# Performance work log

Measured on AMD Instinct MI355X. Metric: run time of the kernel, lower is better.

The kernel has to match this reference:

```python
import jax, jax.numpy as jnp
import numpy as np

HEAD_DIM = 64
KERNEL_EPS = 1e-3  # lucidrains generalized_kernel kernel_epsilon


def setup_inputs() -> dict:
    key = jax.random.key(0)
    k1, k2, k3, k4 = jax.random.split(key, 4)
    B, H, N, D, R = 4, 8, 4096, HEAD_DIM, 256
    return {
        "Q": jax.random.normal(k1, (B, H, N, D), dtype=jnp.float32),
        "K": jax.random.normal(k2, (B, H, N, D), dtype=jnp.float32),
        "V": jax.random.normal(k3, (B, H, N, D), dtype=jnp.float32),
        "mask": jnp.ones((B, N), dtype=jnp.float32),
        "proj": jax.random.normal(k4, (R, D), dtype=jnp.float32),
    }


def reference(Q, K, V, mask, proj):
    # PerformerAttention.forward: scale Q,K by d^{-1/4}, zero out masked keys/values
    scale = 1.0 / jnp.sqrt(jnp.sqrt(jnp.float32(HEAD_DIM)))
    m = mask[:, None, :, None]               # [B,1,N,1]
    q = Q * scale
    k = K * scale * m
    v = V * m

    # generalized random-feature map phi(x) = relu(x @ proj^T) + eps  -> [B,H,N,R]
    phi_q = jax.nn.relu(jnp.einsum('bhnd,rd->bhnr', q, proj)) + KERNEL_EPS
    phi_k = jax.nn.relu(jnp.einsum('bhnd,rd->bhnr', k, proj)) + KERNEL_EPS

    # non-causal linear attention: out = phi_q (phi_k^T v) / (phi_q (phi_k^T 1))
    k_sum = phi_k.sum(axis=2)                                  # [B,H,R]
    d_inv = 1.0 / jnp.einsum('bhnr,bhr->bhn', phi_q, k_sum)    # [B,H,N]
    context = jnp.einsum('bhnr,bhnd->bhrd', phi_k, v)          # [B,H,R,D]
    out = jnp.einsum('bhnr,bhrd->bhnd', phi_q, context) * d_inv[..., None]
    return out
```

## Files before the change

### kernel.cpp

```cpp
#include <hip/hip_runtime.h>
#include <hip/hip_bf16.h>

#define BB 4
#define HH 8
#define NN 4096
#define DD 64
#define RR 256

constexpr float SCALE = 0.35355339059327373f;
constexpr float KEPS  = 0.001f;

typedef __attribute__((ext_vector_type(8)))  short short8;
typedef __attribute__((ext_vector_type(16))) float f32x16;

#define MFMA(a, b, c) __builtin_amdgcn_mfma_f32_32x32x16_bf16(a, b, c, 0, 0, 0)

union S8U { short8 s; uint4 u; };

__device__ inline unsigned bfpk(float a, float b) {
    __hip_bfloat162 h = __float22bfloat162_rn(make_float2(a, b));
    return *reinterpret_cast<unsigned*>(&h);
}
__device__ inline f32x16 fz16() {
    f32x16 z;
#pragma unroll
    for (int e = 0; e < 16; ++e) z[e] = 0.f;
    return z;
}

__global__ __launch_bounds__(256)
void prep_proj(const float* __restrict__ proj, unsigned short* __restrict__ projb)
{
    const int i = (blockIdx.x * 256 + threadIdx.x) * 4;
    const float4 v = *(const float4*)(proj + i);
    uint2 o; o.x = bfpk(v.x * SCALE, v.y * SCALE); o.y = bfpk(v.z * SCALE, v.w * SCALE);
    *(uint2*)(projb + i) = o;
}

__global__ __launch_bounds__(256, 2)
void pk_ctx_kernel(const float* __restrict__ Kmat, const float* __restrict__ Vmat,
                   const float* __restrict__ mask, const unsigned short* __restrict__ projb,
                   float* __restrict__ g_ctxT, float* __restrict__ g_ksum)
{
    __shared__ unsigned short kt[2][32 * 72];
    __shared__ unsigned short vt[2][32 * 68];

    const int tid = threadIdx.x;
    const int w = tid >> 6, lane = tid & 63;
    const int l31 = lane & 31, hf = lane >> 5;
    const int b = blockIdx.z, h = blockIdx.y;
    const int bh = b * HH + h;
    const int n0 = blockIdx.x * 256;

    const int sn = tid >> 3, sc = (tid & 7) * 8;
    const long rowbase = ((long)bh * NN + n0 + sn) * DD + sc;
    const int  mbase   = b * NN + n0 + sn;

    short8 pfrag[2][4];
#pragma unroll
    for (int rt = 0; rt < 2; ++rt)
#pragma unroll
        for (int ks = 0; ks < 4; ++ks)
            pfrag[rt][ks] = *(const short8*)(projb + (w * 64 + rt * 32 + l31) * DD + ks * 16 + hf * 8);

    f32x16 acc[2][2];
    acc[0][0] = fz16(); acc[0][1] = fz16(); acc[1][0] = fz16(); acc[1][1] = fz16();
    float ksum[2] = {0.f, 0.f};

    auto stage = [&](int buf, int sub) {
        const long off = rowbase + (long)sub * 32 * DD;
        const float m = mask[mbase + sub * 32];
        const float4 ka = *(const float4*)(Kmat + off);
        const float4 kc = *(const float4*)(Kmat + off + 4);
        S8U t; t.u = make_uint4(bfpk(ka.x * m, ka.y * m), bfpk(ka.z * m, ka.w * m),
                                bfpk(kc.x * m, kc.y * m), bfpk(kc.z * m, kc.w * m));
        *(short8*)&kt[buf][sn * 72 + sc] = t.s;
        const float4 va = *(const float4*)(Vmat + off);
        const float4 vc = *(const float4*)(Vmat + off + 4);
        *(uint2*)&vt[buf][sn * 68 + sc]     = make_uint2(bfpk(va.x * m, va.y * m), bfpk(va.z * m, va.w * m));
        *(uint2*)&vt[buf][sn * 68 + sc + 4] = make_uint2(bfpk(vc.x * m, vc.y * m), bfpk(vc.z * m, vc.w * m));
    };

    stage(0, 0);
    __syncthreads();

    for (int sub = 0; sub < 8; ++sub) {
        const int buf = sub & 1;
        if (sub < 7) stage(buf ^ 1, sub + 1);

        short8 afr[4];
#pragma unroll
        for (int ks = 0; ks < 4; ++ks)
            afr[ks] = *(const short8*)&kt[buf][l31 * 72 + ks * 16 + hf * 8];

        unsigned own[2][8];
#pragma unroll
        for (int rt = 0; rt < 2; ++rt) {
            f32x16 p = fz16();
#pragma unroll
            for (int ks = 0; ks < 4; ++ks) p = MFMA(afr[ks], pfrag[rt][ks], p);
#pragma unroll
            for (int g = 0; g < 4; ++g) {
                const float p0 = fmaxf(p[4*g+0], 0.f) + KEPS;
                const float p1 = fmaxf(p[4*g+1], 0.f) + KEPS;
                const float p2 = fmaxf(p[4*g+2], 0.f) + KEPS;
                const float p3 = fmaxf(p[4*g+3], 0.f) + KEPS;
                ksum[rt] += (p0 + p1) + (p2 + p3);
                own[rt][2*g]   = bfpk(p0, p1);
                own[rt][2*g+1] = bfpk(p2, p3);
            }
        }
        unsigned par[2][8];
#pragma unroll
        for (int rt = 0; rt < 2; ++rt)
#pragma unroll
            for (int q = 0; q < 8; ++q)
                par[rt][q] = (unsigned)__shfl_xor((int)own[rt][q], 32, 64);

#pragma unroll
        for (int kk = 0; kk < 2; ++kk) {
            S8U bf[2];
#pragma unroll
            for (int rt = 0; rt < 2; ++rt) {
                if (hf == 0) bf[rt].u = make_uint4(own[rt][4*kk],   own[rt][4*kk+1],
                                                   par[rt][4*kk],   par[rt][4*kk+1]);
                else         bf[rt].u = make_uint4(par[rt][4*kk+2], par[rt][4*kk+3],
                                                   own[rt][4*kk+2], own[rt][4*kk+3]);
            }
#pragma unroll
            for (int mt = 0; mt < 2; ++mt) {
                short8 av;
#pragma unroll
                for (int j = 0; j < 8; ++j)
                    av[j] = (short)vt[buf][(kk * 16 + hf * 8 + j) * 68 + mt * 32 + l31];
                acc[mt][0] = MFMA(av, bf[0].s, acc[mt][0]);
                acc[mt][1] = MFMA(av, bf[1].s, acc[mt][1]);
            }
        }
        __syncthreads();
    }

#pragma unroll
    for (int mt = 0; mt < 2; ++mt)
#pragma unroll
        for (int rt = 0; rt < 2; ++rt)
#pragma unroll
            for (int i = 0; i < 16; ++i) {
                const int drow = mt * 32 + (i & 3) + 8 * (i >> 2) + 4 * hf;
                atomicAdd(g_ctxT + ((long)bh * DD + drow) * RR + w * 64 + rt * 32 + l31,
                          acc[mt][rt][i]);
            }
#pragma unroll
    for (int rt = 0; rt < 2; ++rt) {
        const float kst = ksum[rt] + __shfl_xor(ksum[rt], 32, 64);
        if (hf == 0) atomicAdd(g_ksum + bh * RR + w * 64 + rt * 32 + l31, kst);
    }
}

__global__ __launch_bounds__(256)
void finalize_ctx(const float* __restrict__ g_ctxT, unsigned short* __restrict__ ctb)
{
    const long i = ((long)blockIdx.x * 256 + threadIdx.x) * 8;
    const float4 a = *(const float4*)(g_ctxT + i);
    const float4 c = *(const float4*)(g_ctxT + i + 4);
    uint4 o = make_uint4(bfpk(a.x, a.y), bfpk(a.z, a.w), bfpk(c.x, c.y), bfpk(c.z, c.w));
    *(uint4*)(ctb + i) = o;
}

__global__ __launch_bounds__(256, 4)
void out_kernel(const float* __restrict__ Qmat, const unsigned short* __restrict__ projb,
                const unsigned short* __restrict__ ctb, const float* __restrict__ g_ksum,
                float* __restrict__ out)
{
    __shared__ unsigned short pl[256 * 72];
    __shared__ float ks_lds[RR];

    const int tid = threadIdx.x;
    const int w = tid >> 6, lane = tid & 63;
    const int l31 = lane & 31, hf = lane >> 5;
    const int bh = blockIdx.z * HH + blockIdx.y;
    const int n0 = blockIdx.x * 128;
    const int nl = w * 32 + l31;

#pragma unroll
    for (int t = 0; t < 8; ++t) {
        const int u = tid + t * 256;
        const uint4 v = ((const uint4*)projb)[u];
        *(uint4*)&pl[(u >> 3) * 72 + (u & 7) * 8] = v;
    }
    ks_lds[tid] = g_ksum[bh * RR + tid];

    const long qrow = ((long)bh * NN + n0 + nl) * DD;
    short8 qfr[4];
#pragma unroll
    for (int ks = 0; ks < 4; ++ks) {
        const float4 a = *(const float4*)(Qmat + qrow + ks * 16 + hf * 8);
        const float4 c = *(const float4*)(Qmat + qrow + ks * 16 + hf * 8 + 4);
        S8U t; t.u = make_uint4(bfpk(a.x, a.y), bfpk(a.z, a.w), bfpk(c.x, c.y), bfpk(c.z, c.w));
        qfr[ks] = t.s;
    }
    __syncthreads();

    f32x16 cacc[2];
    cacc[0] = fz16(); cacc[1] = fz16();
    float s_acc = 0.f;

    short8 cpre[4];
#pragma unroll
    for (int q = 0; q < 4; ++q)
        cpre[q] = *(const short8*)(ctb + ((long)bh * DD + (q & 1) * 32 + l31) * RR
                                       + (q >> 1) * 16 + hf * 8);

    for (int rt = 0; rt < 8; ++rt) {
        short8 cur[4];
#pragma unroll
        for (int q = 0; q < 4; ++q) cur[q] = cpre[q];
        if (rt < 7) {
#pragma unroll
            for (int q = 0; q < 4; ++q)
                cpre[q] = *(const short8*)(ctb + ((long)bh * DD + (q & 1) * 32 + l31) * RR
                                               + (rt + 1) * 32 + (q >> 1) * 16 + hf * 8);
        }
        f32x16 p = fz16();
#pragma unroll
        for (int ks = 0; ks < 4; ++ks) {
            const short8 af = *(const short8*)&pl[(rt * 32 + l31) * 72 + ks * 16 + hf * 8];
            p = MFMA(af, qfr[ks], p);
        }
        unsigned own[8];
#pragma unroll
        for (int g = 0; g < 4; ++g) {
            const float4 kv = *(const float4*)&ks_lds[rt * 32 + 8 * g + 4 * hf];
            const float p0 = fmaxf(p[4*g+0], 0.f) + KEPS; s_acc = fmaf(p0, kv.x, s_acc);
            const float p1 = fmaxf(p[4*g+1], 0.f) + KEPS; s_acc = fmaf(p1, kv.y, s_acc);
            const float p2 = fmaxf(p[4*g+2], 0.f) + KEPS; s_acc = fmaf(p2, kv.z, s_acc);
            const float p3 = fmaxf(p[4*g+3], 0.f) + KEPS; s_acc = fmaf(p3, kv.w, s_acc);
            own[2*g]   = bfpk(p0, p1);
            own[2*g+1] = bfpk(p2, p3);
        }
        unsigned par[8];
#pragma unroll
        for (int q = 0; q < 8; ++q) par[q] = (unsigned)__shfl_xor((int)own[q], 32, 64);
#pragma unroll
        for (int kk = 0; kk < 2; ++kk) {
            S8U a;
            if (hf == 0) a.u = make_uint4(own[4*kk],   own[4*kk+1], par[4*kk],   par[4*kk+1]);
            else         a.u = make_uint4(par[4*kk+2], par[4*kk+3], own[4*kk+2], own[4*kk+3]);
            cacc[0] = MFMA(a.s, cur[kk * 2 + 0], cacc[0]);
            cacc[1] = MFMA(a.s, cur[kk * 2 + 1], cacc[1]);
        }
    }

    const float st = s_acc + __shfl_xor(s_acc, 32, 64);
    const float sinv = 1.0f / st;
#pragma unroll
    for (int i = 0; i < 16; ++i) {
        const int row = (i & 3) + 8 * (i >> 2) + 4 * hf;
        const float sv = __shfl(sinv, row, 64);
#pragma unroll
        for (int dt = 0; dt < 2; ++dt)
            out[((long)bh * NN + n0 + w * 32 + row) * DD + dt * 32 + l31] = cacc[dt][i] * sv;
    }
}

extern "C" void kernel_launch(void* const* d_in, const int* in_sizes, int n_in,
                              void* d_out, int out_size, void* d_ws, size_t ws_size,
                              hipStream_t stream)
{
    const float* Q    = (const float*)d_in[0];
    const float* K    = (const float*)d_in[1];
    const float* V    = (const float*)d_in[2];
    const float* mask = (const float*)d_in[3];
    const float* proj = (const float*)d_in[4];
    float* out = (float*)d_out;

    float* g_ctxT = (float*)d_ws;
    float* g_ksum = g_ctxT + (size_t)BB * HH * DD * RR;
    unsigned short* projb = (unsigned short*)(g_ksum + (size_t)BB * HH * RR);
    unsigned short* ctb   = projb + (size_t)RR * DD;

    const size_t zbytes = ((size_t)BB * HH * DD * RR + (size_t)BB * HH * RR) * sizeof(float);
    hipMemsetAsync(d_ws, 0, zbytes, stream);

    prep_proj<<<dim3(RR * DD / 1024), 256, 0, stream>>>(proj, projb);

    dim3 g1(NN / 256, HH, BB);
    pk_ctx_kernel<<<g1, 256, 0, stream>>>(K, V, mask, projb, g_ctxT, g_ksum);

    finalize_ctx<<<dim3(BB * HH * DD * RR / 2048), 256, 0, stream>>>(g_ctxT, ctb);

    dim3 g2(NN / 128, HH, BB);
    out_kernel<<<g2, 256, 0, stream>>>(Q, projb, ctb, g_ksum, out);
}
```

Baseline: 221.5 us.

## Split feature dimension across blocks and drop context finalize kernel

The context kernel now splits the 256 random features into two halves across twice as many blocks, so each wave handles one 32-feature tile. This reduces per-thread registers and raises the occupancy target, at the cost of loading and converting K/V twice. The separate bf16 finalize kernel is removed: the output kernel reads fp32 context directly from global memory and converts it inline. The output kernel also reads proj from global instead of staging it in LDS. Together these aim to cut launch overhead and LDS traffic, but they add redundant global loads and conversions in the inner loop.

```diff
diff --git a/kernel.cpp b/kernel.cpp
--- a/kernel.cpp
+++ b/kernel.cpp
@@ -37,7 +37,7 @@
     *(uint2*)(projb + i) = o;
 }
 
-__global__ __launch_bounds__(256, 2)
+__global__ __launch_bounds__(256, 3)
 void pk_ctx_kernel(const float* __restrict__ Kmat, const float* __restrict__ Vmat,
                    const float* __restrict__ mask, const unsigned short* __restrict__ projb,
                    float* __restrict__ g_ctxT, float* __restrict__ g_ksum)
@@ -50,22 +50,22 @@
     const int l31 = lane & 31, hf = lane >> 5;
     const int b = blockIdx.z, h = blockIdx.y;
     const int bh = b * HH + h;
-    const int n0 = blockIdx.x * 256;
+    const int nc = blockIdx.x >> 1, rhalf = blockIdx.x & 1;
+    const int n0 = nc * 256;
+    const int rg = rhalf * 128 + w * 32 + l31;
 
     const int sn = tid >> 3, sc = (tid & 7) * 8;
     const long rowbase = ((long)bh * NN + n0 + sn) * DD + sc;
     const int  mbase   = b * NN + n0 + sn;
 
-    short8 pfrag[2][4];
-#pragma unroll
-    for (int rt = 0; rt < 2; ++rt)
-#pragma unroll
-        for (int ks = 0; ks < 4; ++ks)
-            pfrag[rt][ks] = *(const short8*)(projb + (w * 64 + rt * 32 + l31) * DD + ks * 16 + hf * 8);
-
-    f32x16 acc[2][2];
-    acc[0][0] = fz16(); acc[0][1] = fz16(); acc[1][0] = fz16(); acc[1][1] = fz16();
-    float ksum[2] = {0.f, 0.f};
+    short8 pfrag[4];
+#pragma unroll
+    for (int ks = 0; ks < 4; ++ks)
+        pfrag[ks] = *(const short8*)(projb + rg * DD + ks * 16 + hf * 8);
+
+    f32x16 acc[2];
+    acc[0] = fz16(); acc[1] = fz16();
+    float ksum = 0.f;
 
     auto stage = [&](int buf, int sub) {
         const long off = rowbase + (long)sub * 32 * DD;
@@ -92,49 +92,37 @@
 #pragma unroll
         for (int ks = 0; ks < 4; ++ks)
             afr[ks] = *(const short8*)&kt[buf][l31 * 72 + ks * 16 + hf * 8];
-
-        unsigned own[2][8];
-#pragma unroll
-        for (int rt = 0; rt < 2; ++rt) {
-            f32x16 p = fz16();
-#pragma unroll
-            for (int ks = 0; ks < 4; ++ks) p = MFMA(afr[ks], pfrag[rt][ks], p);
-#pragma unroll
-            for (int g = 0; g < 4; ++g) {
-                const float p0 = fmaxf(p[4*g+0], 0.f) + KEPS;
-                const float p1 = fmaxf(p[4*g+1], 0.f) + KEPS;
-                const float p2 = fmaxf(p[4*g+2], 0.f) + KEPS;
-                const float p3 = fmaxf(p[4*g+3], 0.f) + KEPS;
-                ksum[rt] += (p0 + p1) + (p2 + p3);
-                own[rt][2*g]   = bfpk(p0, p1);
-                own[rt][2*g+1] = bfpk(p2, p3);
-            }
-        }
-        unsigned par[2][8];
-#pragma unroll
-        for (int rt = 0; rt < 2; ++rt)
-#pragma unroll
-            for (int q = 0; q < 8; ++q)
-                par[rt][q] = (unsigned)__shfl_xor((int)own[rt][q], 32, 64);
+        f32x16 p = fz16();
+#pragma unroll
+        for (int ks = 0; ks < 4; ++ks) p = MFMA(afr[ks], pfrag[ks], p);
+
+        unsigned own[8];
+#pragma unroll
+        for (int g = 0; g < 4; ++g) {
+            const float p0 = fmaxf(p[4*g+0], 0.f) + KEPS;
+            const float p1 = fmaxf(p[4*g+1], 0.f) + KEPS;
+            const float p2 = fmaxf(p[4*g+2], 0.f) + KEPS;
+            const float p3 = fmaxf(p[4*g+3], 0.f) + KEPS;
+            ksum += (p0 + p1) + (p2 + p3);
+            own[2*g]   = bfpk(p0, p1);
+            own[2*g+1] = bfpk(p2, p3);
+        }
+        unsigned par[8];
+#pragma unroll
+        for (int q = 0; q < 8; ++q) par[q] = (unsigned)__shfl_xor((int)own[q], 32, 64);
 
 #pragma unroll
         for (int kk = 0; kk < 2; ++kk) {
-            S8U bf[2];
-#pragma unroll
-            for (int rt = 0; rt < 2; ++rt) {
-                if (hf == 0) bf[rt].u = make_uint4(own[rt][4*kk],   own[rt][4*kk+1],
-                                                   par[rt][4*kk],   par[rt][4*kk+1]);
-                else         bf[rt].u = make_uint4(par[rt][4*kk+2], par[rt][4*kk+3],
-                                                   own[rt][4*kk+2], own[rt][4*kk+3]);
-            }
+            S8U bf;
+            if (hf == 0) bf.u = make_uint4(own[4*kk],   own[4*kk+1], par[4*kk],   par[4*kk+1]);
+            else         bf.u = make_uint4(par[4*kk+2], par[4*kk+3], own[4*kk+2], own[4*kk+3]);
 #pragma unroll
             for (int mt = 0; mt < 2; ++mt) {
                 short8 av;
 #pragma unroll
                 for (int j = 0; j < 8; ++j)
                     av[j] = (short)vt[buf][(kk * 16 + hf * 8 + j) * 68 + mt * 32 + l31];
-                acc[mt][0] = MFMA(av, bf[0].s, acc[mt][0]);
-                acc[mt][1] = MFMA(av, bf[1].s, acc[mt][1]);
+                acc[mt] = MFMA(av, bf.s, acc[mt]);
             }
         }
         __syncthreads();
@@ -143,36 +131,20 @@
 #pragma unroll
     for (int mt = 0; mt < 2; ++mt)
 #pragma unroll
-        for (int rt = 0; rt < 2; ++rt)
-#pragma unroll
-            for (int i = 0; i < 16; ++i) {
-                const int drow = mt * 32 + (i & 3) + 8 * (i >> 2) + 4 * hf;
-                atomicAdd(g_ctxT + ((long)bh * DD + drow) * RR + w * 64 + rt * 32 + l31,
-                          acc[mt][rt][i]);
-            }
-#pragma unroll
-    for (int rt = 0; rt < 2; ++rt) {
-        const float kst = ksum[rt] + __shfl_xor(ksum[rt], 32, 64);
-        if (hf == 0) atomicAdd(g_ksum + bh * RR + w * 64 + rt * 32 + l31, kst);
-    }
-}
-
-__global__ __launch_bounds__(256)
-void finalize_ctx(const float* __restrict__ g_ctxT, unsigned short* __restrict__ ctb)
-{
-    const long i = ((long)blockIdx.x * 256 + threadIdx.x) * 8;
-    const float4 a = *(const float4*)(g_ctxT + i);
-    const float4 c = *(const float4*)(g_ctxT + i + 4);
-    uint4 o = make_uint4(bfpk(a.x, a.y), bfpk(a.z, a.w), bfpk(c.x, c.y), bfpk(c.z, c.w));
-    *(uint4*)(ctb + i) = o;
-}
-
-__global__ __launch_bounds__(256, 4)
+        for (int i = 0; i < 16; ++i) {
+            const int drow = mt * 32 + (i & 3) + 8 * (i >> 2) + 4 * hf;
+            atomicAdd(g_ctxT + ((long)bh * DD + drow) * RR + rhalf * 128 + w * 32 + l31,
+                      acc[mt][i]);
+        }
+    const float kst = ksum + __shfl_xor(ksum, 32, 64);
+    if (hf == 0) atomicAdd(g_ksum + bh * RR + rhalf * 128 + w * 32 + l31, kst);
+}
+
+__global__ __launch_bounds__(256, 3)
 void out_kernel(const float* __restrict__ Qmat, const unsigned short* __restrict__ projb,
-                const unsigned short* __restrict__ ctb, const float* __restrict__ g_ksum,
+                const float* __restrict__ g_ctxT, const float* __restrict__ g_ksum,
                 float* __restrict__ out)
 {
-    __shared__ unsigned short pl[256 * 72];
     __shared__ float ks_lds[RR];
 
     const int tid = threadIdx.x;
@@ -182,12 +154,6 @@
     const int n0 = blockIdx.x * 128;
     const int nl = w * 32 + l31;
 
-#pragma unroll
-    for (int t = 0; t < 8; ++t) {
-        const int u = tid + t * 256;
-        const uint4 v = ((const uint4*)projb)[u];
-        *(uint4*)&pl[(u >> 3) * 72 + (u & 7) * 8] = v;
-    }
     ks_lds[tid] = g_ksum[bh * RR + tid];
 
     const long qrow = ((long)bh * NN + n0 + nl) * DD;
@@ -205,26 +171,11 @@
     cacc[0] = fz16(); cacc[1] = fz16();
     float s_acc = 0.f;
 
-    short8 cpre[4];
-#pragma unroll
-    for (int q = 0; q < 4; ++q)
-        cpre[q] = *(const short8*)(ctb + ((long)bh * DD + (q & 1) * 32 + l31) * RR
-                                       + (q >> 1) * 16 + hf * 8);
-
     for (int rt = 0; rt < 8; ++rt) {
-        short8 cur[4];
-#pragma unroll
-        for (int q = 0; q < 4; ++q) cur[q] = cpre[q];
-        if (rt < 7) {
-#pragma unroll
-            for (int q = 0; q < 4; ++q)
-                cpre[q] = *(const short8*)(ctb + ((long)bh * DD + (q & 1) * 32 + l31) * RR
-                                               + (rt + 1) * 32 + (q >> 1) * 16 + hf * 8);
-        }
         f32x16 p = fz16();
 #pragma unroll
         for (int ks = 0; ks < 4; ++ks) {
-            const short8 af = *(const short8*)&pl[(rt * 32 + l31) * 72 + ks * 16 + hf * 8];
+            const short8 af = *(const short8*)(projb + (rt * 32 + l31) * DD + ks * 16 + hf * 8);
             p = MFMA(af, qfr[ks], p);
         }
         unsigned own[8];
@@ -241,13 +192,22 @@
         unsigned par[8];
 #pragma unroll
         for (int q = 0; q < 8; ++q) par[q] = (unsigned)__shfl_xor((int)own[q], 32, 64);
+
 #pragma unroll
         for (int kk = 0; kk < 2; ++kk) {
             S8U a;
             if (hf == 0) a.u = make_uint4(own[4*kk],   own[4*kk+1], par[4*kk],   par[4*kk+1]);
             else         a.u = make_uint4(par[4*kk+2], par[4*kk+3], own[4*kk+2], own[4*kk+3]);
-            cacc[0] = MFMA(a.s, cur[kk * 2 + 0], cacc[0]);
-            cacc[1] = MFMA(a.s, cur[kk * 2 + 1], cacc[1]);
+#pragma unroll
+            for (int dt = 0; dt < 2; ++dt) {
+                const float* cp = g_ctxT + ((long)bh * DD + dt * 32 + l31) * RR
+                                         + rt * 32 + kk * 16 + hf * 8;
+                const float4 x = *(const float4*)cp;
+                const float4 y = *(const float4*)(cp + 4);
+                S8U bfr; bfr.u = make_uint4(bfpk(x.x, x.y), bfpk(x.z, x.w),
+                                            bfpk(y.x, y.y), bfpk(y.z, y.w));
+                cacc[dt] = MFMA(a.s, bfr.s, cacc[dt]);
+            }
         }
     }
 
@@ -277,18 +237,15 @@
     float* g_ctxT = (float*)d_ws;
     float* g_ksum = g_ctxT + (size_t)BB * HH * DD * RR;
     unsigned short* projb = (unsigned short*)(g_ksum + (size_t)BB * HH * RR);
-    unsigned short* ctb   = projb + (size_t)RR * DD;
 
     const size_t zbytes = ((size_t)BB * HH * DD * RR + (size_t)BB * HH * RR) * sizeof(float);
     hipMemsetAsync(d_ws, 0, zbytes, stream);
 
     prep_proj<<<dim3(RR * DD / 1024), 256, 0, stream>>>(proj, projb);
 
-    dim3 g1(NN / 256, HH, BB);
+    dim3 g1((NN / 256) * 2, HH, BB);
     pk_ctx_kernel<<<g1, 256, 0, stream>>>(K, V, mask, projb, g_ctxT, g_ksum);
 
-    finalize_ctx<<<dim3(BB * HH * DD * RR / 2048), 256, 0, stream>>>(g_ctxT, ctb);
-
     dim3 g2(NN / 128, HH, BB);
-    out_kernel<<<g2, 256, 0, stream>>>(Q, projb, ctb, g_ksum, out);
-}
+    out_kernel<<<g2, 256, 0, stream>>>(Q, projb, g_ctxT, g_ksum, out);
+}
```

Result: faster. 209.8 us (-5.3%).
